# Optimization experiments

Hardware: AMD Instinct MI355X
Metric: run time of the kernel (lower is better)

## Reference

```python
import jax, jax.numpy as jnp
import numpy as np

B, L = 2, 2048
D_MODEL = 512
KERNEL = 5
DILATIONS = (1, 2, 4, 8, 1, 2, 4, 8)
HEADS = len(DILATIONS)
HEAD_W = D_MODEL // HEADS
MODE = "center"


def _dilocal_content(x_bedl, kernel, dilations, mode):
    # x_bedl: (B, E, D, L). Returns content in layout (B, L, E, H, K, D),
    # matching LCSA's dilocal + transpose(-4,-1).transpose(-4,-2).transpose(-5,-4).
    Lx = x_bedl.shape[-1]
    per_head = []
    for d in dilations:
        P = (kernel - 1) * d
        if mode == "forward":
            pads = (P, 0)
        elif mode == "backward":
            pads = (0, P)
        else:  # center
            pads = (P // 2, P - P // 2)
        padded = jnp.pad(x_bedl, ((0, 0),) * (x_bedl.ndim - 1) + (pads,))
        win = jnp.stack([padded[..., k * d:k * d + Lx] for k in range(kernel)], axis=-2)
        per_head.append(win)
    c = jnp.stack(per_head, axis=-2)  # (B, E, D, K, H, L)
    return jnp.transpose(c, (0, 5, 1, 4, 3, 2))  # (B, L, E, H, K, D)


def setup_inputs() -> dict:
    key = jax.random.key(0)
    ks = jax.random.split(key, 6)
    s_in = 1.0 / np.sqrt(D_MODEL)
    s_out = 1.0 / np.sqrt(HEADS * HEAD_W)
    x = jax.random.normal(ks[0], (B, L, D_MODEL), jnp.float32)
    q_w = jax.random.normal(ks[1], (1, HEADS, 1, HEAD_W, D_MODEL), jnp.float32) * s_in
    q_b = jnp.zeros((1, HEADS, 1, HEAD_W), jnp.float32)
    k_w = jax.random.normal(ks[2], (1, HEADS, KERNEL, HEAD_W, D_MODEL), jnp.float32) * s_in
    k_b = jnp.zeros((1, HEADS, KERNEL, HEAD_W), jnp.float32)
    v_w = jax.random.normal(ks[3], (1, HEADS, KERNEL, HEAD_W, D_MODEL), jnp.float32) * s_in
    v_b = jnp.zeros((1, HEADS, KERNEL, HEAD_W), jnp.float32)
    o_w = jax.random.normal(ks[4], (1, D_MODEL, HEADS * HEAD_W), jnp.float32) * s_out
    o_b = jnp.zeros((1, D_MODEL), jnp.float32)
    return {"x": x, "q_w": q_w, "q_b": q_b, "k_w": k_w, "k_b": k_b,
            "v_w": v_w, "v_b": v_b, "o_w": o_w, "o_b": o_b}


def reference(x, q_w, q_b, k_w, k_b, v_w, v_b, o_w, o_b) -> jnp.ndarray:
    b, l, _ = x.shape
    # ensemble=None path: unsqueeze(-3) then transpose(-2,-1) -> (B, E=1, D, L)
    t = jnp.swapaxes(x[:, None, :, :], -2, -1)
    content = _dilocal_content(t, KERNEL, DILATIONS, MODE)  # (B, L, 1, H, K, D)
    # query uses kernel_width=1 (no padding, dilation irrelevant): (B, L, 1, H, 1, D)
    query = jnp.broadcast_to(x[:, :, None, None, None, :], (b, l, 1, HEADS, 1, D_MODEL))
    # per-(head, kernel-position) projections
    q = jnp.einsum('blehkd,ehkod->blehko', query, q_w) + q_b      # (B,L,1,H,1,O)
    k = jnp.einsum('blehkd,ehkod->blehko', content, k_w) + k_b    # (B,L,1,H,K,O)
    v = jnp.einsum('blehkd,ehkod->blehko', content, v_w) + v_b    # (B,L,1,H,K,O)
    logits = jnp.einsum('blehqo,blehko->blehqk', q, k)            # (B,L,1,H,1,K)
    score = jax.nn.softmax(logits, axis=-1)
    attn = jnp.einsum('blehqk,blehko->blehqo', score, v) / jnp.sqrt(jnp.float32(HEAD_W))
    attn = attn[..., 0, :]                                        # squeeze(-2) -> (B,L,1,H,O)
    flat = attn.reshape(b, l, 1, HEADS * HEAD_W)
    out = jnp.einsum('blef,eof->bleo', flat, o_w) + o_b           # (B,L,1,D)
    # transpose(-3,-2) then squeeze ensemble -> (B, L, D)
    return out[:, :, 0, :]
```

## Files before the change

### kernel.cpp

```cpp
#include <hip/hip_runtime.h>
#include <hip/hip_bf16.h>

using bf16 = __hip_bfloat16;
typedef __attribute__((ext_vector_type(8))) short short8;
typedef __attribute__((ext_vector_type(4))) float f32x4;

__device__ __constant__ int c_dil[8] = {1, 2, 4, 8, 1, 2, 4, 8};

__device__ inline void store1(float* p, float v) { *p = v; }
__device__ inline void store1(bf16* p, float v) { *p = __float2bfloat16(v); }

__device__ inline void gload_lds16(const void* g, void* l) {
    __builtin_amdgcn_global_load_lds(
        (const __attribute__((address_space(1))) unsigned int*)g,
        (__attribute__((address_space(3))) unsigned int*)l, 16, 0, 0);
}

template <int N> __device__ inline void vwait() {
    asm volatile("s_waitcnt vmcnt(%0)" :: "n"(N) : "memory");
}
__device__ inline void lgkm0_fence() {
    asm volatile("s_waitcnt lgkmcnt(0)" ::: "memory");
    __builtin_amdgcn_sched_barrier(0);
}
__device__ inline void barrier_pin() {
    __builtin_amdgcn_s_barrier();
    __builtin_amdgcn_sched_barrier(0);
}

__device__ inline unsigned short f2bf(float f) {
    const unsigned u = __float_as_uint(f);
    return (unsigned short)((u + 0x7fffu + ((u >> 16) & 1u)) >> 16);
}
__device__ inline float bf2f(unsigned short h) { return __uint_as_float(((unsigned)h) << 16); }

__device__ inline void conv_block(const float* __restrict__ src, bf16* __restrict__ dst,
                                  int ld, int mode, int idx) {
    const float4 v = *reinterpret_cast<const float4*>(src + idx);
    const int r = idx >> 9, c = idx & 511;
    bf16* d = dst + (size_t)r * ld + c;
    const float vv[4] = {v.x, v.y, v.z, v.w};
    ushort4 hi, lo;
    unsigned short* hp = &hi.x; unsigned short* lp = &lo.x;
#pragma unroll
    for (int j = 0; j < 4; ++j) {
        hp[j] = f2bf(vv[j]);
        lp[j] = f2bf(vv[j] - bf2f(hp[j]));
    }
    *reinterpret_cast<ushort4*>(d) = hi;
    if (mode == 1) *reinterpret_cast<ushort4*>(d + 512) = lo;
    else if (mode == 2) *reinterpret_cast<ushort4*>(d + 512) = hi;
}

__global__ __launch_bounds__(256) void conv_all(
    const float* __restrict__ x,  const float* __restrict__ qw, const float* __restrict__ kw,
    const float* __restrict__ vw, const float* __restrict__ ow,
    const float* __restrict__ qb, const float* __restrict__ kb,
    bf16* A2, bf16* Wqk, bf16* Wv, bf16* Wo, float* bqk)
{
    const int b = blockIdx.x, t = threadIdx.x;
    if (b < 2048)       conv_block(x,  A2,                       1024, 1, (b * 256 + t) * 4);
    else if (b < 2304)  conv_block(qw, Wqk,                      1024, 2, ((b - 2048) * 256 + t) * 4);
    else if (b < 3584)  conv_block(kw, Wqk + (size_t)512 * 1024, 1024, 2, ((b - 2304) * 256 + t) * 4);
    else if (b < 4864)  conv_block(vw, Wv,                        512, 0, ((b - 3584) * 256 + t) * 4);
    else if (b < 5120)  conv_block(ow, Wo,                        512, 0, ((b - 4864) * 256 + t) * 4);
    else { const int i = (b - 5120) * 256 + t; bqk[i] = (i < 512) ? qb[i] : kb[i - 512]; }
}

template <int NB>
__device__ __forceinline__ void run_tile(
    short* AsB, short* BsB,
    const bf16* __restrict__ A, int lda,
    const bf16* __restrict__ W, int ldw,
    const float* __restrict__ bias,
    bf16* __restrict__ C, int ldc,
    int bm, int bn, int nsteps)
{
    constexpr int ASTRIDE = 256 * 64;
    constexpr int BSTRIDE = 320 * 64;
    const int tid = threadIdx.x, wid = tid >> 6, lane = tid & 63;

    const int sslot = ((tid & 7) ^ ((tid >> 3) & 7)) << 4;
    const char* pA[4];
    const char* pB[NB];
#pragma unroll
    for (int i = 0; i < 4; ++i)
        pA[i] = (const char*)A + (size_t)(bm + i * 64 + (tid >> 3)) * lda * 2 + sslot;
#pragma unroll
    for (int i = 0; i < NB; ++i)
        pB[i] = (const char*)W + (size_t)(bn + i * 64 + (tid >> 3)) * ldw * 2 + sslot;

    auto stageA = [&](int kt1) {
        char* d = (char*)(AsB + (kt1 & 1) * ASTRIDE);
#pragma unroll
        for (int i = 0; i < 4; ++i) { gload_lds16(pA[i], d + i * 8192 + wid * 1024); pA[i] += 128; }
    };
    auto stageB = [&](int kt1) {
        char* d = (char*)(BsB + (kt1 & 1) * BSTRIDE);
#pragma unroll
        for (int i = 0; i < NB; ++i) { gload_lds16(pB[i], d + i * 8192 + wid * 1024); pB[i] += 128; }
    };

    f32x4 acc[8][NB];
#pragma unroll
    for (int m = 0; m < 8; ++m)
#pragma unroll
        for (int n = 0; n < NB; ++n) acc[m][n] = f32x4{0.f, 0.f, 0.f, 0.f};

    const int lr16 = lane & 15;
    const int hi8  = (lane >> 4) * 8;
    const int swz  = (lr16 & 7) << 3;
    const int k0   = hi8 ^ swz;
    const int k1   = (32 + hi8) ^ swz;
    const int wrM = wid >> 2, wcN = wid & 3;
    const int arow0 = wrM * 128 + lr16;
    const int brow0 = wcN * (NB * 16) + lr16;

    stageA(0); stageB(0);
    vwait<0>();
    barrier_pin();

    for (int kt = 0; kt < nsteps; ++kt) {
        const short* a  = AsB + (kt & 1) * ASTRIDE;
        const short* bb = BsB + (kt & 1) * BSTRIDE;
        const bool pf = (kt + 1 < nsteps);
        short8 af[4], bw0[NB], bw1[NB];

#pragma unroll
        for (int m = 0; m < 4; ++m) af[m] = *(const short8*)&a[(arow0 + m * 16) * 64 + k0];
#pragma unroll
        for (int n = 0; n < NB; ++n) bw0[n] = *(const short8*)&bb[(brow0 + n * 16) * 64 + k0];
        if (pf) stageA(kt + 1);
        barrier_pin();
        lgkm0_fence();
        __builtin_amdgcn_s_setprio(1);
#pragma unroll
        for (int m = 0; m < 4; ++m)
#pragma unroll
            for (int n = 0; n < NB; ++n)
                acc[m][n] = __builtin_amdgcn_mfma_f32_16x16x32_bf16(af[m], bw0[n], acc[m][n], 0, 0, 0);
        __builtin_amdgcn_s_setprio(0);
        barrier_pin();

#pragma unroll
        for (int m = 0; m < 4; ++m) af[m] = *(const short8*)&a[(arow0 + 64 + m * 16) * 64 + k0];
        if (pf) stageB(kt + 1);
        barrier_pin();
        lgkm0_fence();
        __builtin_amdgcn_s_setprio(1);
#pragma unroll
        for (int m = 0; m < 4; ++m)
#pragma unroll
            for (int n = 0; n < NB; ++n)
                acc[4 + m][n] = __builtin_amdgcn_mfma_f32_16x16x32_bf16(af[m], bw0[n], acc[4 + m][n], 0, 0, 0);
        __builtin_amdgcn_s_setprio(0);
        barrier_pin();

#pragma unroll
        for (int m = 0; m < 4; ++m) af[m] = *(const short8*)&a[(arow0 + m * 16) * 64 + k1];
#pragma unroll
        for (int n = 0; n < NB; ++n) bw1[n] = *(const short8*)&bb[(brow0 + n * 16) * 64 + k1];
        barrier_pin();
        lgkm0_fence();
        __builtin_amdgcn_s_setprio(1);
#pragma unroll
        for (int m = 0; m < 4; ++m)
#pragma unroll
            for (int n = 0; n < NB; ++n)
                acc[m][n] = __builtin_amdgcn_mfma_f32_16x16x32_bf16(af[m], bw1[n], acc[m][n], 0, 0, 0);
        __builtin_amdgcn_s_setprio(0);
        barrier_pin();

#pragma unroll
        for (int m = 0; m < 4; ++m) af[m] = *(const short8*)&a[(arow0 + 64 + m * 16) * 64 + k1];
        barrier_pin();
        lgkm0_fence();
        __builtin_amdgcn_s_setprio(1);
#pragma unroll
        for (int m = 0; m < 4; ++m)
#pragma unroll
            for (int n = 0; n < NB; ++n)
                acc[4 + m][n] = __builtin_amdgcn_mfma_f32_16x16x32_bf16(af[m], bw1[n], acc[4 + m][n], 0, 0, 0);
        __builtin_amdgcn_s_setprio(0);
        vwait<0>();
        barrier_pin();
    }

    const int r4 = (lane >> 4) * 4;
#pragma unroll
    for (int m = 0; m < 8; ++m) {
#pragma unroll
        for (int n = 0; n < NB; ++n) {
            const int col = bn + wcN * (NB * 16) + n * 16 + lr16;
            const float bv = bias[col];
#pragma unroll
            for (int jj = 0; jj < 4; ++jj) {
                const int row = bm + wrM * 128 + m * 16 + r4 + jj;
                store1(C + (size_t)row * ldc + col, acc[m][n][jj] + bv);
            }
        }
    }
}

__global__ __launch_bounds__(512, 1) void gemm8p(
    const bf16* __restrict__ A,
    const bf16* __restrict__ Wqk, const float* __restrict__ bqk, bf16* __restrict__ PQK,
    const bf16* __restrict__ Wv,  const float* __restrict__ vb,  bf16* __restrict__ PV)
{
    __shared__ short As[2 * 256 * 64];
    __shared__ short Bs[2 * 320 * 64];

    const int b = blockIdx.x;
    if (b < 192) {
        const int xcd = b & 7, i = b >> 3;
        const int by = xcd * 2 + (i & 1), bx = i >> 1;
        run_tile<4>(As, Bs, A, 1024, Wqk, 1024, bqk, PQK, 3072, by * 256, bx * 256, 16);
    } else {
        const int v = b - 192;
        const int xcd = v & 7, i = v >> 3;
        const int by = xcd * 2 + (i & 1), bx = i >> 1;
        run_tile<5>(As, Bs, A, 1024, Wv, 512, vb, PV, 2560, by * 256, bx * 320, 8);
    }
}

template <int BN, typename TC>
__global__ __launch_bounds__(256) void gemm128(
    const bf16* __restrict__ A, int lda, int cw, int rpx,
    const bf16* __restrict__ W0, int ldw0, const float* __restrict__ b0,
    TC* __restrict__ C0, int ldc0, int nt0, int nx0)
{
    constexpr int NF = BN / 32;
    constexpr int NLOAD = (BN == 128) ? 4 : 3;
    __shared__ short As[4][128 * 32];
    __shared__ short Bs[4][BN * 32];

    const int tid = threadIdx.x, wid = tid >> 6, lane = tid & 63;

    const int xcd = (int)blockIdx.x & 7;
    const int i   = (int)blockIdx.x >> 3;
    const int grp = rpx * cw;
    const int cc = i / grp, w2 = i % grp;
    const int rr = w2 / cw, c = w2 % cw;
    const int bx = cc * cw + c;
    const int by = xcd * rpx + rr;

    const int bm = by * 128;
    const int bn = bx * BN;
    const int nsteps = nt0;

    const int srow = lane >> 2;
    const int ssw  = (((lane & 3) ^ ((lane >> 3) & 3)) << 4);
    const char* pA0 = (const char*)A + (size_t)(bm + wid * 16 + srow) * lda * 2 + ssw;
    const char* pA1 = pA0 + (size_t)64 * lda * 2;
    const char* pB0 = (const char*)W0 + (size_t)(bn + wid * 16 + srow) * ldw0 * 2 + ssw;

    f32x4 acc[4][NF];
#pragma unroll
    for (int m = 0; m < 4; ++m)
#pragma unroll
        for (int n = 0; n < NF; ++n) acc[m][n] = f32x4{0.f, 0.f, 0.f, 0.f};

    const int lr16 = lane & 15;
    const int wsw8 = (((lane >> 4) ^ ((lr16 >> 1) & 3)) << 3);
    const int wr = wid >> 1, wc = wid & 1;
    int offA[4], offB[NF];
#pragma unroll
    for (int m = 0; m < 4; ++m) offA[m] = (wr * 4 + m) * 512 + lr16 * 32 + wsw8;
#pragma unroll
    for (int n = 0; n < NF; ++n) offB[n] = (wc * NF + n) * 512 + lr16 * 32 + wsw8;

    auto stage = [&](int buf) {
        gload_lds16(pA0, (char*)As[buf] + wid * 1024);
        gload_lds16(pA1, (char*)As[buf] + (wid + 4) * 1024);
        gload_lds16(pB0, (char*)Bs[buf] + wid * 1024);
        pA0 += 64; pA1 += 64; pB0 += 64;
    };

    stage(0);
    stage(1);
    stage(2);

    for (int s = 0; s < nsteps; ++s) {
        const int cur = s & 3;
        if (s + 3 < nsteps) {
            stage((s + 3) & 3);
            vwait<3 * NLOAD>();
        } else if (s + 2 < nsteps) {
            vwait<2 * NLOAD>();
        } else if (s + 1 < nsteps) {
            vwait<NLOAD>();
        } else {
            vwait<0>();
        }
        barrier_pin();

        short8 af[4], bw[NF];
#pragma unroll
        for (int m = 0; m < 4; ++m)
            af[m] = *(const short8*)&As[cur][offA[m]];
#pragma unroll
        for (int n = 0; n < NF; ++n)
            bw[n] = *(const short8*)&Bs[cur][offB[n]];

        __builtin_amdgcn_s_setprio(1);
#pragma unroll
        for (int m = 0; m < 4; ++m)
#pragma unroll
            for (int n = 0; n < NF; ++n)
                acc[m][n] = __builtin_amdgcn_mfma_f32_16x16x32_bf16(af[m], bw[n], acc[m][n], 0, 0, 0);
        __builtin_amdgcn_s_setprio(0);

        barrier_pin();
    }

    const int r4 = (lane >> 4) * 4;
#pragma unroll
    for (int m = 0; m < 4; ++m) {
#pragma unroll
        for (int n = 0; n < NF; ++n) {
            const int col = bn + wc * (NF * 16) + n * 16 + lr16;
            const float bv = b0[col];
#pragma unroll
            for (int jj = 0; jj < 4; ++jj) {
                const int row = bm + wr * 64 + m * 16 + r4 + jj;
                store1(C0 + (size_t)row * ldc0 + col, acc[m][n][jj] + bv);
            }
        }
    }
}

__global__ __launch_bounds__(256) void attn_k(
    const bf16* __restrict__ PQK, const bf16* __restrict__ PV, bf16* __restrict__ Aout)
{
    const int lane = threadIdx.x & 63;
    const int wave = threadIdx.x >> 6;
    const int task = blockIdx.x * 4 + wave;
    const int h  = task & 7;
    const int bl = task >> 3;
    const int l  = bl & 2047;
    const int d  = c_dil[h];

    const float q = __bfloat162float(PQK[(size_t)bl * 3072 + h * 64 + lane]);

    float logits[5], vvals[5];
#pragma unroll
    for (int kk = 0; kk < 5; ++kk) {
        const int pos = l + (kk - 2) * d;
        const bool ok = (pos >= 0) && (pos < 2048);
        float kv = 0.f, vv = 0.f;
        if (ok) {
            const size_t rb = (size_t)(bl - l + pos);
            kv = __bfloat162float(PQK[rb * 3072 + 512 + (h * 5 + kk) * 64 + lane]);
            vv = __bfloat162float(PV[rb * 2560 + (h * 5 + kk) * 64 + lane]);
        }
        vvals[kk] = vv;
        float lg = q * kv;
#pragma unroll
        for (int s = 32; s; s >>= 1) lg += __shfl_xor(lg, s);
        logits[kk] = lg;
    }

    float mx = logits[0];
#pragma unroll
    for (int kk = 1; kk < 5; ++kk) mx = fmaxf(mx, logits[kk]);
    float e[5], ssum = 0.f;
#pragma unroll
    for (int kk = 0; kk < 5; ++kk) { e[kk] = __expf(logits[kk] - mx); ssum += e[kk]; }
    float acc = 0.f;
#pragma unroll
    for (int kk = 0; kk < 5; ++kk) acc += e[kk] * vvals[kk];
    acc *= 0.125f / ssum;

    Aout[(size_t)bl * 512 + h * 64 + lane] = __float2bfloat16(acc);
}

extern "C" void kernel_launch(void* const* d_in, const int* in_sizes, int n_in,
                              void* d_out, int out_size, void* d_ws, size_t ws_size,
                              hipStream_t stream)
{
    const float* x   = (const float*)d_in[0];
    const float* q_w = (const float*)d_in[1];
    const float* q_b = (const float*)d_in[2];
    const float* k_w = (const float*)d_in[3];
    const float* k_b = (const float*)d_in[4];
    const float* v_w = (const float*)d_in[5];
    const float* v_b = (const float*)d_in[6];
    const float* o_w = (const float*)d_in[7];
    const float* o_b = (const float*)d_in[8];
    float* out = (float*)d_out;

    const int M = 4096;

    char* p = (char*)d_ws;
    bf16* A2  = (bf16*)p;  p += (size_t)M * 1024 * 2;
    bf16* Wqk = (bf16*)p;  p += (size_t)3072 * 1024 * 2;
    bf16* Wv  = (bf16*)p;  p += (size_t)2560 * 512 * 2;
    bf16* Wo  = (bf16*)p;  p += (size_t)512 * 512 * 2;
    float* bqk = (float*)p; p += 3072 * 4;
    bf16* PQK = (bf16*)p;  p += (size_t)M * 3072 * 2;
    bf16* PV  = (bf16*)p;
    bf16* Aout = A2;

    conv_all<<<dim3(5132), dim3(256), 0, stream>>>(x, q_w, k_w, v_w, o_w, q_b, k_b,
                                                   A2, Wqk, Wv, Wo, bqk);
    gemm8p<<<dim3(320), dim3(512), 0, stream>>>(A2, Wqk, bqk, PQK, Wv, v_b, PV);
    attn_k<<<dim3(8192), dim3(256), 0, stream>>>(PQK, PV, Aout);
    gemm128<64, float><<<dim3(256), dim3(256), 0, stream>>>(
        Aout, 512, 8, 4,
        Wo, 512, o_b, out, 512, 16, 8);
}
```

Baseline: 88.00 us.

## Reuse single bf16 weight tile across hi/lo activation halves in QK GEMM

Split-bf16 emulation of the QK projection used to concatenate A=[hi|lo] against W=[hi|hi], duplicating the weight matrix along K. Now the weight is stored once (K=512), and a dedicated run_qk routine loads each weight tile once into shared memory and multiplies it with both the hi and lo activation tiles. This halves weight conversion writes and weight global traffic for the QK GEMM. In exchange the pipeline is more intricate: it has more barriers per step, a single-buffered B tile, and a shared-memory union that raises the LDS footprint.

```diff
diff --git a/kernel.cpp b/kernel.cpp
--- a/kernel.cpp
+++ b/kernel.cpp
@@ -18,6 +18,7 @@
 
 template <int N> __device__ inline void vwait() {
     asm volatile("s_waitcnt vmcnt(%0)" :: "n"(N) : "memory");
+    __builtin_amdgcn_sched_barrier(0);
 }
 __device__ inline void lgkm0_fence() {
     asm volatile("s_waitcnt lgkmcnt(0)" ::: "memory");
@@ -49,7 +50,6 @@
     }
     *reinterpret_cast<ushort4*>(d) = hi;
     if (mode == 1) *reinterpret_cast<ushort4*>(d + 512) = lo;
-    else if (mode == 2) *reinterpret_cast<ushort4*>(d + 512) = hi;
 }
 
 __global__ __launch_bounds__(256) void conv_all(
@@ -59,36 +59,181 @@
     bf16* A2, bf16* Wqk, bf16* Wv, bf16* Wo, float* bqk)
 {
     const int b = blockIdx.x, t = threadIdx.x;
-    if (b < 2048)       conv_block(x,  A2,                       1024, 1, (b * 256 + t) * 4);
-    else if (b < 2304)  conv_block(qw, Wqk,                      1024, 2, ((b - 2048) * 256 + t) * 4);
-    else if (b < 3584)  conv_block(kw, Wqk + (size_t)512 * 1024, 1024, 2, ((b - 2304) * 256 + t) * 4);
-    else if (b < 4864)  conv_block(vw, Wv,                        512, 0, ((b - 3584) * 256 + t) * 4);
-    else if (b < 5120)  conv_block(ow, Wo,                        512, 0, ((b - 4864) * 256 + t) * 4);
+    if (b < 2048)       conv_block(x,  A2,                      1024, 1, (b * 256 + t) * 4);
+    else if (b < 2304)  conv_block(qw, Wqk,                      512, 0, ((b - 2048) * 256 + t) * 4);
+    else if (b < 3584)  conv_block(kw, Wqk + (size_t)512 * 512,  512, 0, ((b - 2304) * 256 + t) * 4);
+    else if (b < 4864)  conv_block(vw, Wv,                       512, 0, ((b - 3584) * 256 + t) * 4);
+    else if (b < 5120)  conv_block(ow, Wo,                       512, 0, ((b - 4864) * 256 + t) * 4);
     else { const int i = (b - 5120) * 256 + t; bqk[i] = (i < 512) ? qb[i] : kb[i - 512]; }
 }
 
-template <int NB>
-__device__ __forceinline__ void run_tile(
-    short* AsB, short* BsB,
-    const bf16* __restrict__ A, int lda,
-    const bf16* __restrict__ W, int ldw,
+__device__ __forceinline__ void run_qk(
+    short* smem,
+    const bf16* __restrict__ A,
+    const bf16* __restrict__ W,
     const float* __restrict__ bias,
-    bf16* __restrict__ C, int ldc,
-    int bm, int bn, int nsteps)
-{
+    bf16* __restrict__ C,
+    int bm, int bn)
+{
+    short* Ahi[2] = { smem,          smem + 16384 };
+    short* Alo[2] = { smem + 32768,  smem + 49152 };
+    short* Bb     =   smem + 65536;
+
+    const int tid = threadIdx.x, wid = tid >> 6, lane = tid & 63;
+
+    const int sslot = ((tid & 7) ^ ((tid >> 3) & 7)) << 4;
+    const char* pAh[4];
+    const char* pAl[4];
+    const char* pB[4];
+#pragma unroll
+    for (int i = 0; i < 4; ++i) {
+        const int row = i * 64 + (tid >> 3);
+        pAh[i] = (const char*)A + (size_t)(bm + row) * 2048 + sslot;
+        pAl[i] = pAh[i] + 1024;
+        pB[i]  = (const char*)W + (size_t)(bn + row) * 1024 + sslot;
+    }
+
+    auto stageAhi = [&](int s1) {
+        char* d = (char*)Ahi[s1 & 1];
+#pragma unroll
+        for (int i = 0; i < 4; ++i) { gload_lds16(pAh[i], d + i * 8192 + wid * 1024); pAh[i] += 128; }
+    };
+    auto stageAlo = [&](int s1) {
+        char* d = (char*)Alo[s1 & 1];
+#pragma unroll
+        for (int i = 0; i < 4; ++i) { gload_lds16(pAl[i], d + i * 8192 + wid * 1024); pAl[i] += 128; }
+    };
+    auto stageB = [&]() {
+        char* d = (char*)Bb;
+#pragma unroll
+        for (int i = 0; i < 4; ++i) { gload_lds16(pB[i], d + i * 8192 + wid * 1024); pB[i] += 128; }
+    };
+
+    f32x4 acc[8][4];
+#pragma unroll
+    for (int m = 0; m < 8; ++m)
+#pragma unroll
+        for (int n = 0; n < 4; ++n) acc[m][n] = f32x4{0.f, 0.f, 0.f, 0.f};
+
+    const int lr16 = lane & 15;
+    const int hi8  = (lane >> 4) * 8;
+    const int swz  = (lr16 & 7) << 3;
+    const int k0   = hi8 ^ swz;
+    const int k1   = (32 + hi8) ^ swz;
+    const int wrM = wid >> 2, wcN = wid & 3;
+    const int arow0 = wrM * 128 + lr16;
+    const int brow0 = wcN * 64 + lr16;
+
+    stageAhi(0); stageB(); stageAlo(0);
+    vwait<4>();
+    barrier_pin();
+
+    short8 af[8], bw0[4], bw1[4];
+    for (int s = 0; s < 8; ++s) {
+        const short* ah = Ahi[s & 1];
+        const short* al = Alo[s & 1];
+        const bool pf = (s < 7);
+
+#pragma unroll
+        for (int m = 0; m < 8; ++m) af[m] = *(const short8*)&ah[(arow0 + m * 16) * 64 + k0];
+#pragma unroll
+        for (int n = 0; n < 4; ++n) bw0[n] = *(const short8*)&Bb[(brow0 + n * 16) * 64 + k0];
+        lgkm0_fence();
+        barrier_pin();
+        if (pf) stageAhi(s + 1);
+        __builtin_amdgcn_s_setprio(1);
+#pragma unroll
+        for (int m = 0; m < 8; ++m)
+#pragma unroll
+            for (int n = 0; n < 4; ++n)
+                acc[m][n] = __builtin_amdgcn_mfma_f32_16x16x32_bf16(af[m], bw0[n], acc[m][n], 0, 0, 0);
+        __builtin_amdgcn_s_setprio(0);
+
+#pragma unroll
+        for (int m = 0; m < 8; ++m) af[m] = *(const short8*)&ah[(arow0 + m * 16) * 64 + k1];
+#pragma unroll
+        for (int n = 0; n < 4; ++n) bw1[n] = *(const short8*)&Bb[(brow0 + n * 16) * 64 + k1];
+        lgkm0_fence();
+        if (pf) vwait<4>(); else vwait<0>();
+        barrier_pin();
+        if (pf) stageB();
+        __builtin_amdgcn_s_setprio(1);
+#pragma unroll
+        for (int m = 0; m < 8; ++m)
+#pragma unroll
+            for (int n = 0; n < 4; ++n)
+                acc[m][n] = __builtin_amdgcn_mfma_f32_16x16x32_bf16(af[m], bw1[n], acc[m][n], 0, 0, 0);
+        __builtin_amdgcn_s_setprio(0);
+
+#pragma unroll
+        for (int m = 0; m < 8; ++m) af[m] = *(const short8*)&al[(arow0 + m * 16) * 64 + k0];
+        lgkm0_fence();
+        barrier_pin();
+        if (pf) stageAlo(s + 1);
+        __builtin_amdgcn_s_setprio(1);
+#pragma unroll
+        for (int m = 0; m < 8; ++m)
+#pragma unroll
+            for (int n = 0; n < 4; ++n)
+                acc[m][n] = __builtin_amdgcn_mfma_f32_16x16x32_bf16(af[m], bw0[n], acc[m][n], 0, 0, 0);
+        __builtin_amdgcn_s_setprio(0);
+
+#pragma unroll
+        for (int m = 0; m < 8; ++m) af[m] = *(const short8*)&al[(arow0 + m * 16) * 64 + k1];
+        lgkm0_fence();
+        vwait<4>();
+        barrier_pin();
+        __builtin_amdgcn_s_setprio(1);
+#pragma unroll
+        for (int m = 0; m < 8; ++m)
+#pragma unroll
+            for (int n = 0; n < 4; ++n)
+                acc[m][n] = __builtin_amdgcn_mfma_f32_16x16x32_bf16(af[m], bw1[n], acc[m][n], 0, 0, 0);
+        __builtin_amdgcn_s_setprio(0);
+        barrier_pin();
+    }
+
+    const int r4 = (lane >> 4) * 4;
+#pragma unroll
+    for (int m = 0; m < 8; ++m) {
+#pragma unroll
+        for (int n = 0; n < 4; ++n) {
+            const int col = bn + wcN * 64 + n * 16 + lr16;
+            const float bv = bias[col];
+#pragma unroll
+            for (int jj = 0; jj < 4; ++jj) {
+                const int row = bm + wrM * 128 + m * 16 + r4 + jj;
+                store1(C + (size_t)row * 3072 + col, acc[m][n][jj] + bv);
+            }
+        }
+    }
+}
+
+__device__ __forceinline__ void run_v(
+    short* smem,
+    const bf16* __restrict__ A,
+    const bf16* __restrict__ W,
+    const float* __restrict__ bias,
+    bf16* __restrict__ C,
+    int bm, int bn)
+{
+    constexpr int NB = 5;
+    short* AsB = smem;
+    short* BsB = smem + 32768;
     constexpr int ASTRIDE = 256 * 64;
     constexpr int BSTRIDE = 320 * 64;
     const int tid = threadIdx.x, wid = tid >> 6, lane = tid & 63;
+    const int nsteps = 8;
 
     const int sslot = ((tid & 7) ^ ((tid >> 3) & 7)) << 4;
     const char* pA[4];
     const char* pB[NB];
 #pragma unroll
     for (int i = 0; i < 4; ++i)
-        pA[i] = (const char*)A + (size_t)(bm + i * 64 + (tid >> 3)) * lda * 2 + sslot;
+        pA[i] = (const char*)A + (size_t)(bm + i * 64 + (tid >> 3)) * 2048 + sslot;
 #pragma unroll
     for (int i = 0; i < NB; ++i)
-        pB[i] = (const char*)W + (size_t)(bn + i * 64 + (tid >> 3)) * ldw * 2 + sslot;
+        pB[i] = (const char*)W + (size_t)(bn + i * 64 + (tid >> 3)) * 1024 + sslot;
 
     auto stageA = [&](int kt1) {
         char* d = (char*)(AsB + (kt1 & 1) * ASTRIDE);
@@ -196,7 +341,7 @@
 #pragma unroll
             for (int jj = 0; jj < 4; ++jj) {
                 const int row = bm + wrM * 128 + m * 16 + r4 + jj;
-                store1(C + (size_t)row * ldc + col, acc[m][n][jj] + bv);
+                store1(C + (size_t)row * 2560 + col, acc[m][n][jj] + bv);
             }
         }
     }
@@ -207,19 +352,17 @@
     const bf16* __restrict__ Wqk, const float* __restrict__ bqk, bf16* __restrict__ PQK,
     const bf16* __restrict__ Wv,  const float* __restrict__ vb,  bf16* __restrict__ PV)
 {
-    __shared__ short As[2 * 256 * 64];
-    __shared__ short Bs[2 * 320 * 64];
-
+    __shared__ short smem[81920];
     const int b = blockIdx.x;
     if (b < 192) {
         const int xcd = b & 7, i = b >> 3;
         const int by = xcd * 2 + (i & 1), bx = i >> 1;
-        run_tile<4>(As, Bs, A, 1024, Wqk, 1024, bqk, PQK, 3072, by * 256, bx * 256, 16);
+        run_qk(smem, A, Wqk, bqk, PQK, by * 256, bx * 256);
     } else {
         const int v = b - 192;
         const int xcd = v & 7, i = v >> 3;
         const int by = xcd * 2 + (i & 1), bx = i >> 1;
-        run_tile<5>(As, Bs, A, 1024, Wv, 512, vb, PV, 2560, by * 256, bx * 320, 8);
+        run_v(smem, A, Wv, vb, PV, by * 256, bx * 320);
     }
 }
 
@@ -393,7 +536,7 @@
 
     char* p = (char*)d_ws;
     bf16* A2  = (bf16*)p;  p += (size_t)M * 1024 * 2;
-    bf16* Wqk = (bf16*)p;  p += (size_t)3072 * 1024 * 2;
+    bf16* Wqk = (bf16*)p;  p += (size_t)3072 * 512 * 2;
     bf16* Wv  = (bf16*)p;  p += (size_t)2560 * 512 * 2;
     bf16* Wo  = (bf16*)p;  p += (size_t)512 * 512 * 2;
     float* bqk = (float*)p; p += 3072 * 4;
```

New measurement: 84.56 us. 3.9% less time.

## Restructure QKV GEMM with smaller tiles, shared weight fragments for hi/lo split

Applied to the files above, without the earlier changes.

The QK projection previously multiplied a K=1024 concatenated [x_hi|x_lo] input by duplicated weights. It now reads the bf16 weights once (K=512) and issues two MFMAs per B fragment, one for the hi A slice and one for the lo A slice. This halves the weight conversion writes and the B-tile loads. Tiles shrink to 128x384 for QK and 128x256 for V, launching 576 blocks with room for several resident per CU (launch bounds 512,4). The K loop uses 32-wide steps, a two-stage prefetch, and a single barrier pair per step instead of four sub-phases, trading larger per-tile reuse for more parallelism and overlap.

```diff
diff --git a/kernel.cpp b/kernel.cpp
--- a/kernel.cpp
+++ b/kernel.cpp
@@ -18,6 +18,7 @@
 
 template <int N> __device__ inline void vwait() {
     asm volatile("s_waitcnt vmcnt(%0)" :: "n"(N) : "memory");
+    __builtin_amdgcn_sched_barrier(0);
 }
 __device__ inline void lgkm0_fence() {
     asm volatile("s_waitcnt lgkmcnt(0)" ::: "memory");
@@ -49,7 +50,6 @@
     }
     *reinterpret_cast<ushort4*>(d) = hi;
     if (mode == 1) *reinterpret_cast<ushort4*>(d + 512) = lo;
-    else if (mode == 2) *reinterpret_cast<ushort4*>(d + 512) = hi;
 }
 
 __global__ __launch_bounds__(256) void conv_all(
@@ -59,167 +59,217 @@
     bf16* A2, bf16* Wqk, bf16* Wv, bf16* Wo, float* bqk)
 {
     const int b = blockIdx.x, t = threadIdx.x;
-    if (b < 2048)       conv_block(x,  A2,                       1024, 1, (b * 256 + t) * 4);
-    else if (b < 2304)  conv_block(qw, Wqk,                      1024, 2, ((b - 2048) * 256 + t) * 4);
-    else if (b < 3584)  conv_block(kw, Wqk + (size_t)512 * 1024, 1024, 2, ((b - 2304) * 256 + t) * 4);
-    else if (b < 4864)  conv_block(vw, Wv,                        512, 0, ((b - 3584) * 256 + t) * 4);
-    else if (b < 5120)  conv_block(ow, Wo,                        512, 0, ((b - 4864) * 256 + t) * 4);
+    if (b < 2048)       conv_block(x,  A2,                      1024, 1, (b * 256 + t) * 4);
+    else if (b < 2304)  conv_block(qw, Wqk,                      512, 0, ((b - 2048) * 256 + t) * 4);
+    else if (b < 3584)  conv_block(kw, Wqk + (size_t)512 * 512,  512, 0, ((b - 2304) * 256 + t) * 4);
+    else if (b < 4864)  conv_block(vw, Wv,                       512, 0, ((b - 3584) * 256 + t) * 4);
+    else if (b < 5120)  conv_block(ow, Wo,                       512, 0, ((b - 4864) * 256 + t) * 4);
     else { const int i = (b - 5120) * 256 + t; bqk[i] = (i < 512) ? qb[i] : kb[i - 512]; }
 }
 
-template <int NB>
-__device__ __forceinline__ void run_tile(
-    short* AsB, short* BsB,
-    const bf16* __restrict__ A, int lda,
-    const bf16* __restrict__ W, int ldw,
+
+__device__ __forceinline__ void run_qk(
+    short* smem,
+    const bf16* __restrict__ A,
+    const bf16* __restrict__ W,
     const float* __restrict__ bias,
-    bf16* __restrict__ C, int ldc,
-    int bm, int bn, int nsteps)
-{
-    constexpr int ASTRIDE = 256 * 64;
-    constexpr int BSTRIDE = 320 * 64;
+    bf16* __restrict__ C,
+    int bm, int bn)
+{
+    short* Ahi = smem;
+    short* Alo = smem + 8192;
+    short* Bb  = smem + 16384;
+
     const int tid = threadIdx.x, wid = tid >> 6, lane = tid & 63;
-
-    const int sslot = ((tid & 7) ^ ((tid >> 3) & 7)) << 4;
-    const char* pA[4];
-    const char* pB[NB];
-#pragma unroll
-    for (int i = 0; i < 4; ++i)
-        pA[i] = (const char*)A + (size_t)(bm + i * 64 + (tid >> 3)) * lda * 2 + sslot;
-#pragma unroll
-    for (int i = 0; i < NB; ++i)
-        pB[i] = (const char*)W + (size_t)(bn + i * 64 + (tid >> 3)) * ldw * 2 + sslot;
-
-    auto stageA = [&](int kt1) {
-        char* d = (char*)(AsB + (kt1 & 1) * ASTRIDE);
-#pragma unroll
-        for (int i = 0; i < 4; ++i) { gload_lds16(pA[i], d + i * 8192 + wid * 1024); pA[i] += 128; }
+    constexpr int NSTEPS = 16;
+
+    const int sslot = (((tid & 3) ^ ((tid >> 3) & 3)) << 4);
+    const char* pAh = (const char*)A + (size_t)(bm + (tid >> 2)) * 2048 + sslot;
+    const char* pAl = pAh + 1024;
+    const char* pB[3];
+#pragma unroll
+    for (int j = 0; j < 3; ++j)
+        pB[j] = (const char*)W + (size_t)(bn + j * 128 + (tid >> 2)) * 1024 + sslot;
+
+    auto stage = [&](int kt) {
+        char* da = (char*)(Ahi + (kt & 1) * 4096);
+        char* dl = (char*)(Alo + (kt & 1) * 4096);
+        char* db = (char*)(Bb  + (kt & 1) * 12288);
+        gload_lds16(pAh, da + wid * 1024); pAh += 64;
+        gload_lds16(pAl, dl + wid * 1024); pAl += 64;
+#pragma unroll
+        for (int j = 0; j < 3; ++j) { gload_lds16(pB[j], db + j * 8192 + wid * 1024); pB[j] += 64; }
     };
-    auto stageB = [&](int kt1) {
-        char* d = (char*)(BsB + (kt1 & 1) * BSTRIDE);
-#pragma unroll
-        for (int i = 0; i < NB; ++i) { gload_lds16(pB[i], d + i * 8192 + wid * 1024); pB[i] += 128; }
+
+    f32x4 acc[4][6];
+#pragma unroll
+    for (int m = 0; m < 4; ++m)
+#pragma unroll
+        for (int n = 0; n < 6; ++n) acc[m][n] = f32x4{0.f, 0.f, 0.f, 0.f};
+
+    const int lr16 = lane & 15;
+    const int koff = (((lane >> 4) ^ ((lr16 >> 1) & 3)) << 3);
+    const int wrM = wid >> 2, wcN = wid & 3;
+    const int arow0 = wrM * 64 + lr16;
+    const int brow0 = wcN * 96 + lr16;
+
+    stage(0);
+    stage(1);
+
+    for (int kt = 0; kt < NSTEPS; ++kt) {
+        if (kt + 1 < NSTEPS) vwait<5>(); else vwait<0>();
+        barrier_pin();
+
+        const short* ah = Ahi + (kt & 1) * 4096;
+        const short* al = Alo + (kt & 1) * 4096;
+        const short* bb = Bb  + (kt & 1) * 12288;
+        short8 fh[4], fl[4], bw[6];
+#pragma unroll
+        for (int m = 0; m < 4; ++m) {
+            fh[m] = *(const short8*)&ah[(arow0 + m * 16) * 32 + koff];
+            fl[m] = *(const short8*)&al[(arow0 + m * 16) * 32 + koff];
+        }
+#pragma unroll
+        for (int n = 0; n < 6; ++n)
+            bw[n] = *(const short8*)&bb[(brow0 + n * 16) * 32 + koff];
+        lgkm0_fence();
+        barrier_pin();
+
+        if (kt + 2 < NSTEPS) stage(kt + 2);
+
+        __builtin_amdgcn_s_setprio(1);
+#pragma unroll
+        for (int m = 0; m < 4; ++m)
+#pragma unroll
+            for (int n = 0; n < 6; ++n)
+                acc[m][n] = __builtin_amdgcn_mfma_f32_16x16x32_bf16(fh[m], bw[n], acc[m][n], 0, 0, 0);
+#pragma unroll
+        for (int m = 0; m < 4; ++m)
+#pragma unroll
+            for (int n = 0; n < 6; ++n)
+                acc[m][n] = __builtin_amdgcn_mfma_f32_16x16x32_bf16(fl[m], bw[n], acc[m][n], 0, 0, 0);
+        __builtin_amdgcn_s_setprio(0);
+    }
+
+    const int r4 = (lane >> 4) * 4;
+#pragma unroll
+    for (int m = 0; m < 4; ++m) {
+#pragma unroll
+        for (int n = 0; n < 6; ++n) {
+            const int col = bn + wcN * 96 + n * 16 + lr16;
+            const float bv = bias[col];
+#pragma unroll
+            for (int jj = 0; jj < 4; ++jj) {
+                const int row = bm + wrM * 64 + m * 16 + r4 + jj;
+                store1(C + (size_t)row * 3072 + col, acc[m][n][jj] + bv);
+            }
+        }
+    }
+}
+
+__device__ __forceinline__ void run_v(
+    short* smem,
+    const bf16* __restrict__ A,
+    const bf16* __restrict__ W,
+    const float* __restrict__ bias,
+    bf16* __restrict__ C,
+    int bm, int bn)
+{
+    short* As = smem;
+    short* Bs = smem + 8192;
+
+    const int tid = threadIdx.x, wid = tid >> 6, lane = tid & 63;
+    constexpr int NSTEPS = 16;
+
+    const int sslot = (((tid & 3) ^ ((tid >> 3) & 3)) << 4);
+    const char* pA = (const char*)A + (size_t)(bm + (tid >> 2)) * 2048 + sslot;
+    const char* pB[2];
+#pragma unroll
+    for (int j = 0; j < 2; ++j)
+        pB[j] = (const char*)W + (size_t)(bn + j * 128 + (tid >> 2)) * 1024 + sslot;
+
+    auto stage = [&](int kt) {
+        char* da = (char*)(As + (kt & 1) * 4096);
+        char* db = (char*)(Bs + (kt & 1) * 8192);
+        gload_lds16(pA, da + wid * 1024); pA += 64;
+#pragma unroll
+        for (int j = 0; j < 2; ++j) { gload_lds16(pB[j], db + j * 8192 + wid * 1024); pB[j] += 64; }
     };
 
-    f32x4 acc[8][NB];
-#pragma unroll
-    for (int m = 0; m < 8; ++m)
-#pragma unroll
-        for (int n = 0; n < NB; ++n) acc[m][n] = f32x4{0.f, 0.f, 0.f, 0.f};
+    f32x4 acc[4][4];
+#pragma unroll
+    for (int m = 0; m < 4; ++m)
+#pragma unroll
+        for (int n = 0; n < 4; ++n) acc[m][n] = f32x4{0.f, 0.f, 0.f, 0.f};
 
     const int lr16 = lane & 15;
-    const int hi8  = (lane >> 4) * 8;
-    const int swz  = (lr16 & 7) << 3;
-    const int k0   = hi8 ^ swz;
-    const int k1   = (32 + hi8) ^ swz;
+    const int koff = (((lane >> 4) ^ ((lr16 >> 1) & 3)) << 3);
     const int wrM = wid >> 2, wcN = wid & 3;
-    const int arow0 = wrM * 128 + lr16;
-    const int brow0 = wcN * (NB * 16) + lr16;
-
-    stageA(0); stageB(0);
-    vwait<0>();
-    barrier_pin();
-
-    for (int kt = 0; kt < nsteps; ++kt) {
-        const short* a  = AsB + (kt & 1) * ASTRIDE;
-        const short* bb = BsB + (kt & 1) * BSTRIDE;
-        const bool pf = (kt + 1 < nsteps);
-        short8 af[4], bw0[NB], bw1[NB];
-
-#pragma unroll
-        for (int m = 0; m < 4; ++m) af[m] = *(const short8*)&a[(arow0 + m * 16) * 64 + k0];
-#pragma unroll
-        for (int n = 0; n < NB; ++n) bw0[n] = *(const short8*)&bb[(brow0 + n * 16) * 64 + k0];
-        if (pf) stageA(kt + 1);
-        barrier_pin();
+    const int arow0 = wrM * 64 + lr16;
+    const int brow0 = wcN * 64 + lr16;
+
+    stage(0);
+    stage(1);
+
+    for (int kt = 0; kt < NSTEPS; ++kt) {
+        if (kt + 1 < NSTEPS) vwait<3>(); else vwait<0>();
+        barrier_pin();
+
+        const short* a  = As + (kt & 1) * 4096;
+        const short* bb = Bs + (kt & 1) * 8192;
+        short8 af[4], bw[4];
+#pragma unroll
+        for (int m = 0; m < 4; ++m)
+            af[m] = *(const short8*)&a[(arow0 + m * 16) * 32 + koff];
+#pragma unroll
+        for (int n = 0; n < 4; ++n)
+            bw[n] = *(const short8*)&bb[(brow0 + n * 16) * 32 + koff];
         lgkm0_fence();
+        barrier_pin();
+
+        if (kt + 2 < NSTEPS) stage(kt + 2);
+
         __builtin_amdgcn_s_setprio(1);
 #pragma unroll
         for (int m = 0; m < 4; ++m)
 #pragma unroll
-            for (int n = 0; n < NB; ++n)
-                acc[m][n] = __builtin_amdgcn_mfma_f32_16x16x32_bf16(af[m], bw0[n], acc[m][n], 0, 0, 0);
+            for (int n = 0; n < 4; ++n)
+                acc[m][n] = __builtin_amdgcn_mfma_f32_16x16x32_bf16(af[m], bw[n], acc[m][n], 0, 0, 0);
         __builtin_amdgcn_s_setprio(0);
-        barrier_pin();
-
-#pragma unroll
-        for (int m = 0; m < 4; ++m) af[m] = *(const short8*)&a[(arow0 + 64 + m * 16) * 64 + k0];
-        if (pf) stageB(kt + 1);
-        barrier_pin();
-        lgkm0_fence();
-        __builtin_amdgcn_s_setprio(1);
-#pragma unroll
-        for (int m = 0; m < 4; ++m)
-#pragma unroll
-            for (int n = 0; n < NB; ++n)
-                acc[4 + m][n] = __builtin_amdgcn_mfma_f32_16x16x32_bf16(af[m], bw0[n], acc[4 + m][n], 0, 0, 0);
-        __builtin_amdgcn_s_setprio(0);
-        barrier_pin();
-
-#pragma unroll
-        for (int m = 0; m < 4; ++m) af[m] = *(const short8*)&a[(arow0 + m * 16) * 64 + k1];
-#pragma unroll
-        for (int n = 0; n < NB; ++n) bw1[n] = *(const short8*)&bb[(brow0 + n * 16) * 64 + k1];
-        barrier_pin();
-        lgkm0_fence();
-        __builtin_amdgcn_s_setprio(1);
-#pragma unroll
-        for (int m = 0; m < 4; ++m)
-#pragma unroll
-            for (int n = 0; n < NB; ++n)
-                acc[m][n] = __builtin_amdgcn_mfma_f32_16x16x32_bf16(af[m], bw1[n], acc[m][n], 0, 0, 0);
-        __builtin_amdgcn_s_setprio(0);
-        barrier_pin();
-
-#pragma unroll
-        for (int m = 0; m < 4; ++m) af[m] = *(const short8*)&a[(arow0 + 64 + m * 16) * 64 + k1];
-        barrier_pin();
-        lgkm0_fence();
-        __builtin_amdgcn_s_setprio(1);
-#pragma unroll
-        for (int m = 0; m < 4; ++m)
-#pragma unroll
-            for (int n = 0; n < NB; ++n)
-                acc[4 + m][n] = __builtin_amdgcn_mfma_f32_16x16x32_bf16(af[m], bw1[n], acc[4 + m][n], 0, 0, 0);
-        __builtin_amdgcn_s_setprio(0);
-        vwait<0>();
-        barrier_pin();
     }
 
     const int r4 = (lane >> 4) * 4;
 #pragma unroll
-    for (int m = 0; m < 8; ++m) {
-#pragma unroll
-        for (int n = 0; n < NB; ++n) {
-            const int col = bn + wcN * (NB * 16) + n * 16 + lr16;
+    for (int m = 0; m < 4; ++m) {
+#pragma unroll
+        for (int n = 0; n < 4; ++n) {
+            const int col = bn + wcN * 64 + n * 16 + lr16;
             const float bv = bias[col];
 #pragma unroll
             for (int jj = 0; jj < 4; ++jj) {
-                const int row = bm + wrM * 128 + m * 16 + r4 + jj;
-                store1(C + (size_t)row * ldc + col, acc[m][n][jj] + bv);
+                const int row = bm + wrM * 64 + m * 16 + r4 + jj;
+                store1(C + (size_t)row * 2560 + col, acc[m][n][jj] + bv);
             }
         }
     }
 }
 
-__global__ __launch_bounds__(512, 1) void gemm8p(
+__global__ __launch_bounds__(512, 4) void gemm_qkv(
     const bf16* __restrict__ A,
     const bf16* __restrict__ Wqk, const float* __restrict__ bqk, bf16* __restrict__ PQK,
     const bf16* __restrict__ Wv,  const float* __restrict__ vb,  bf16* __restrict__ PV)
 {
-    __shared__ short As[2 * 256 * 64];
-    __shared__ short Bs[2 * 320 * 64];
-
+    __shared__ short smem[40960];
     const int b = blockIdx.x;
-    if (b < 192) {
+    if (b < 256) {
         const int xcd = b & 7, i = b >> 3;
-        const int by = xcd * 2 + (i & 1), bx = i >> 1;
-        run_tile<4>(As, Bs, A, 1024, Wqk, 1024, bqk, PQK, 3072, by * 256, bx * 256, 16);
+        const int by = xcd * 4 + (i & 3), bx = i >> 2;
+        run_qk(smem, A, Wqk, bqk, PQK, by * 128, bx * 384);
     } else {
-        const int v = b - 192;
+        const int v = b - 256;
         const int xcd = v & 7, i = v >> 3;
-        const int by = xcd * 2 + (i & 1), bx = i >> 1;
-        run_tile<5>(As, Bs, A, 1024, Wv, 512, vb, PV, 2560, by * 256, bx * 320, 8);
+        const int by = xcd * 4 + (i & 3), bx = i >> 2;
+        run_v(smem, A, Wv, vb, PV, by * 128, bx * 256);
     }
 }
 
@@ -393,7 +443,7 @@
 
     char* p = (char*)d_ws;
     bf16* A2  = (bf16*)p;  p += (size_t)M * 1024 * 2;
-    bf16* Wqk = (bf16*)p;  p += (size_t)3072 * 1024 * 2;
+    bf16* Wqk = (bf16*)p;  p += (size_t)3072 * 512 * 2;
     bf16* Wv  = (bf16*)p;  p += (size_t)2560 * 512 * 2;
     bf16* Wo  = (bf16*)p;  p += (size_t)512 * 512 * 2;
     float* bqk = (float*)p; p += 3072 * 4;
@@ -403,7 +453,7 @@
 
     conv_all<<<dim3(5132), dim3(256), 0, stream>>>(x, q_w, k_w, v_w, o_w, q_b, k_b,
                                                    A2, Wqk, Wv, Wo, bqk);
-    gemm8p<<<dim3(320), dim3(512), 0, stream>>>(A2, Wqk, bqk, PQK, Wv, v_b, PV);
+    gemm_qkv<<<dim3(576), dim3(512), 0, stream>>>(A2, Wqk, bqk, PQK, Wv, v_b, PV);
     attn_k<<<dim3(8192), dim3(256), 0, stream>>>(PQK, PV, Aout);
     gemm128<64, float><<<dim3(256), dim3(256), 0, stream>>>(
         Aout, 512, 8, 4,
```

New measurement: 195.6 us. 2.22x slower.
